# Optimization experiments

Hardware: AMD Instinct MI355X
Metric: run time of the kernel (lower is better)

Reference implementation:

```python
import jax, jax.numpy as jnp
import numpy as np

N = 1024       # sentence length (words incl. root at index 0)
WD = 300       # word embedding dim (GloVe-style)
PD = 25        # pos_emb_dim
H = 125        # hidden_dim_lstm
FC = 100       # hidden_dim_fc
PVOCAB = 50    # POS tagset size


def setup_inputs() -> dict:
    key = jax.random.key(0)
    ks = jax.random.split(key, 14)
    f = lambda k, s: jax.random.normal(k, s, dtype=jnp.float32) * 0.1
    d_in = WD + PD
    return {
        "word_vecs": jax.random.normal(ks[0], (N, WD), dtype=jnp.float32),
        "pos_idx": jax.random.randint(ks[1], (N,), 0, PVOCAB),
        "parents_ids": jax.random.randint(ks[2], (N,), 0, N),
        "pos_emb": f(ks[3], (PVOCAB, PD)),
        "Wih0": f(ks[4], (2, 4 * H, d_in)),
        "Whh0": f(ks[5], (2, 4 * H, H)),
        "b0": f(ks[6], (2, 4 * H)),
        "Wih1": f(ks[7], (2, 4 * H, 2 * H)),
        "Whh1": f(ks[8], (2, 4 * H, H)),
        "b1": f(ks[9], (2, 4 * H)),
        "fc1_W": f(ks[10], (FC, 4 * H)),
        "fc1_b": f(ks[11], (FC,)),
        "fc2_W": f(ks[12], (1, FC)),
        "fc2_b": f(ks[13], (1,)),
    }


def _lstm_dir(x, Wih, Whh, b, reverse):
    # torch LSTM cell, gate order (i, f, g, o); b = b_ih + b_hh
    Hd = Whh.shape[1]
    def step(carry, xt):
        h, c = carry
        g = xt @ Wih.T + h @ Whh.T + b
        i, fg, gg, o = jnp.split(g, 4)
        i = jax.nn.sigmoid(i)
        fg = jax.nn.sigmoid(fg)
        gg = jnp.tanh(gg)
        o = jax.nn.sigmoid(o)
        c = fg * c + i * gg
        h = o * jnp.tanh(c)
        return (h, c), h
    init = (jnp.zeros((Hd,), x.dtype), jnp.zeros((Hd,), x.dtype))
    _, hs = jax.lax.scan(step, init, x, reverse=reverse)
    return hs  # [n, H], already in original time order


def _bilstm_layer(x, Wih, Whh, b):
    hf = _lstm_dir(x, Wih[0], Whh[0], b[0], False)
    hb = _lstm_dir(x, Wih[1], Whh[1], b[1], True)
    return jnp.concatenate([hf, hb], axis=1)  # [n, 2H]


def reference(word_vecs, pos_idx, parents_ids, pos_emb, Wih0, Whh0, b0,
              Wih1, Whh1, b1, fc1_W, fc1_b, fc2_W, fc2_b):
    # encoder: concat word + pos embeddings, 2-layer BiLSTM
    x = jnp.concatenate([word_vecs, pos_emb[pos_idx]], axis=1)  # [n, WD+PD]
    h = _bilstm_layer(x, Wih0, Whh0, b0)
    h = _bilstm_layer(h, Wih1, Whh1, b1)  # [n, 2H]
    n = h.shape[0]
    twoH = h.shape[1]
    # fc1(cat(h_i, h_j)) = h_i @ W_head^T + h_j @ W_child^T + b  (vectorized over all pairs)
    A = h @ fc1_W[:, :twoH].T   # head contribution  [n, FC]
    B = h @ fc1_W[:, twoH:].T   # child contribution [n, FC]
    T = jnp.tanh(A[:, None, :] + B[None, :, :] + fc1_b)  # [n, n, FC]
    raw = T @ fc2_W[0] + fc2_b[0]                         # [n, n]
    ii = jnp.arange(n)
    # original loop skips diagonal and arcs into the root (j == 0); those stay 0
    mask = (ii[:, None] != ii[None, :]) & (ii[None, :] != 0)
    scores_mat = jnp.where(mask, raw, jnp.float32(0.0))
    logits = scores_mat.T  # row j = scores of heads for child j
    logp = jax.nn.log_softmax(logits, axis=1)
    loss = -jnp.mean(logp[jnp.arange(n), parents_ids])
    return loss, scores_mat
```

## Files before the change

kernel.cpp:

```cpp
#include <hip/hip_runtime.h>

typedef float v2f __attribute__((ext_vector_type(2)));

#define LOG2E 1.4426950408889634f
#define LN2   0.6931471805599453f

__device__ __forceinline__ float fexp2(float x) {
  float r; asm("v_exp_f32 %0, %1" : "=v"(r) : "v"(x)); return r;
}
__device__ __forceinline__ float frcp(float x) {
  float r; asm("v_rcp_f32 %0, %1" : "=v"(r) : "v"(x)); return r;
}
__device__ __forceinline__ float flog2(float x) {
  float r; asm("v_log_f32 %0, %1" : "=v"(r) : "v"(x)); return r;
}
__device__ __forceinline__ float dpp_xor1(float v) {
  return __builtin_bit_cast(float,
      __builtin_amdgcn_update_dpp(0, __builtin_bit_cast(int, v), 0xB1, 0xF, 0xF, true));
}
__device__ __forceinline__ float dpp_xor2(float v) {
  return __builtin_bit_cast(float,
      __builtin_amdgcn_update_dpp(0, __builtin_bit_cast(int, v), 0x4E, 0xF, 0xF, true));
}

__global__ void k_embed(const float* __restrict__ wv, const int* __restrict__ pidx,
                        const float* __restrict__ pemb, float* __restrict__ X) {
  int t = blockIdx.x;
  int pi = pidx[t];
  for (int c = threadIdx.x; c < 336; c += 128) {
    float v;
    if (c < 300)      v = wv[t * 300 + c];
    else if (c < 325) v = pemb[pi * 25 + (c - 300)];
    else              v = 0.f;
    X[t * 336 + c] = v;
  }
}

__global__ void k_repack(const float* __restrict__ src, float* __restrict__ dst,
                         int sK, int dK) {
  int r = blockIdx.x;
  for (int c = threadIdx.x; c < dK; c += 128)
    dst[r * dK + c] = (c < sK) ? src[r * sK + c] : 0.f;
}

__global__ void k_wab(const float* __restrict__ fc1W, float* __restrict__ Wab) {
  int r = blockIdx.x;
  int sr = (r < 100) ? r : r - 100;
  int so = (r < 100) ? 0 : 250;
  for (int c = threadIdx.x; c < 256; c += 128)
    Wab[r * 256 + c] = (c < 250) ? fc1W[sr * 500 + so + c] : 0.f;
}

__global__ void k_misc(const float* __restrict__ fc1b, const float* __restrict__ fc2W,
                       float* __restrict__ biasAB, float* __restrict__ sumw) {
  __shared__ float red[128];
  int t = threadIdx.x;
  for (int c = t; c < 256; c += 128)
    biasAB[c] = (c < 100) ? fc1b[c] : 0.f;
  float s = (t < 100) ? fc2W[t] : 0.f;
  red[t] = s; __syncthreads();
  for (int off = 64; off; off >>= 1) {
    if (t < off) red[t] += red[t + off];
    __syncthreads();
  }
  if (t == 0) sumw[0] = red[0];
}

#define BM 64
#define BN 64
#define BKK 16
__global__ __launch_bounds__(256) void k_gemm(
    const float* __restrict__ A, const float* __restrict__ Bw,
    const float* __restrict__ bias, float* __restrict__ C,
    int M, int N, int K, int ldC, long sBz, long sCz, long sbz, int transOut) {
  const int z = blockIdx.z;
  const float* Bp = Bw + (size_t)z * sBz;
  const float* bp = bias + (size_t)z * sbz;
  float* Cp = C + (size_t)z * sCz;
  const int bm = blockIdx.y * BM, bn = blockIdx.x * BN;
  __shared__ __align__(16) float As[BKK][BM + 4];
  __shared__ __align__(16) float Bs[BKK][BN + 4];
  __shared__ float Ts[BN][BM + 1];
  const int tid = threadIdx.x;
  const int tx = tid & 15, ty = tid >> 4;
  const int lr = tid >> 2;
  const int lk = (tid & 3) * 4;
  float acc[4][4];
#pragma unroll
  for (int a = 0; a < 4; ++a)
#pragma unroll
    for (int b = 0; b < 4; ++b) acc[a][b] = 0.f;

  int brow = bn + lr; if (brow >= N) brow = N - 1;
  for (int k0 = 0; k0 < K; k0 += BKK) {
    float4 a4 = *(const float4*)(A + (size_t)(bm + lr) * K + k0 + lk);
    float4 b4 = *(const float4*)(Bp + (size_t)brow * K + k0 + lk);
    __syncthreads();
    As[lk + 0][lr] = a4.x; As[lk + 1][lr] = a4.y; As[lk + 2][lr] = a4.z; As[lk + 3][lr] = a4.w;
    Bs[lk + 0][lr] = b4.x; Bs[lk + 1][lr] = b4.y; Bs[lk + 2][lr] = b4.z; Bs[lk + 3][lr] = b4.w;
    __syncthreads();
#pragma unroll
    for (int kk = 0; kk < BKK; ++kk) {
      float4 av = *(const float4*)&As[kk][ty * 4];
      float4 bv = *(const float4*)&Bs[kk][tx * 4];
      float aa[4] = {av.x, av.y, av.z, av.w};
      float bb[4] = {bv.x, bv.y, bv.z, bv.w};
#pragma unroll
      for (int a = 0; a < 4; ++a)
#pragma unroll
        for (int b = 0; b < 4; ++b)
          acc[a][b] = __builtin_fmaf(aa[a], bb[b], acc[a][b]);
    }
  }
  if (!transOut) {
#pragma unroll
    for (int a = 0; a < 4; ++a) {
      int i = bm + ty * 4 + a;
#pragma unroll
      for (int b = 0; b < 4; ++b) {
        int j = bn + tx * 4 + b;
        if (j < N) Cp[(size_t)i * ldC + j] = acc[a][b] + bp[j];
      }
    }
  } else {
    __syncthreads();
#pragma unroll
    for (int a = 0; a < 4; ++a)
#pragma unroll
      for (int b = 0; b < 4; ++b) {
        int jn = bn + tx * 4 + b; if (jn >= N) jn = N - 1;
        Ts[tx * 4 + b][ty * 4 + a] = acc[a][b] + bp[jn];
      }
    __syncthreads();
    const int n2 = tid >> 2, mq = (tid & 3) * 16;
    const int n = bn + n2;
    if (n < N) {
#pragma unroll
      for (int r = 0; r < 4; ++r) {
        int m0 = mq + r * 4;
        float4 v;
        v.x = Ts[n2][m0 + 0]; v.y = Ts[n2][m0 + 1];
        v.z = Ts[n2][m0 + 2]; v.w = Ts[n2][m0 + 3];
        *(float4*)(Cp + (size_t)n * ldC + bm + m0) = v;
      }
    }
  }
}

__global__ __launch_bounds__(512, 2) void k_rec(const float* __restrict__ Pt,
                                                const float* __restrict__ Whh,
                                                float* __restrict__ hout) {
  const int d = blockIdx.x;
  const bool fwd = (d == 0);
  const int t = threadIdx.x;
  int u = t >> 2; const bool active = (u < 125); if (u > 124) u = 124;
  const int sub = t & 3;

  const float* Wd = Whh + (size_t)d * 500 * 125;
  v2f w[4][16];
#pragma unroll
  for (int g = 0; g < 4; ++g) {
    const float* wr = Wd + (size_t)(g * 125 + u) * 125;
#pragma unroll
    for (int j = 0; j < 16; ++j) {
      int col = sub * 32 + 2 * j;
      v2f ww;
      ww.x = (col     < 125) ? wr[col]     : 0.f;
      ww.y = (col + 1 < 125) ? wr[col + 1] : 0.f;
      w[g][j] = ww;
    }
  }

  __shared__ __align__(16) float hb[2][160];
  __shared__ float hist[32][128];
  for (int i = t; i < 320; i += 512) ((float*)hb)[i] = 0.f;

  const int prow = sub * 125 + u;
  const float4* Pr = (const float4*)(Pt + (size_t)d * 500 * 1024 + (size_t)prow * 1024);

  const float sM = (sub == 2) ? 2.f : 1.f;
  const float sA = (sub == 2) ? 2.f : 1.f;
  const float sB = (sub == 2) ? -1.f : 0.f;
  const bool m0s = (sub == 0), m1s = (sub == 1), m2s = (sub == 2);

  float cst = 0.f;
  float4 cura = Pr[fwd ? 0 : 254];
  float4 curb = Pr[fwd ? 1 : 255];
  __syncthreads();

  for (int cb = 0; cb < 128; ++cb) {
    int nc = (cb + 1 < 128) ? cb + 1 : cb;
    float4 nxta = Pr[fwd ? 2 * nc     : 254 - 2 * nc];
    float4 nxtb = Pr[fwd ? 2 * nc + 1 : 255 - 2 * nc];
#pragma unroll
    for (int e = 0; e < 8; ++e) {
      const int buf = e & 1;
      float pf = (e == 0) ? cura.x : (e == 1) ? cura.y : (e == 2) ? cura.z : (e == 3) ? cura.w
               : (e == 4) ? curb.x : (e == 5) ? curb.y : (e == 6) ? curb.z : curb.w;
      float pb = (e == 0) ? curb.w : (e == 1) ? curb.z : (e == 2) ? curb.y : (e == 3) ? curb.x
               : (e == 4) ? cura.w : (e == 5) ? cura.z : (e == 6) ? cura.y : cura.x;
      float pre = fwd ? pf : pb;
      const float4* hp = (const float4*)&hb[buf][36 * sub];
      v2f a0 = {0.f, 0.f}, a1 = {0.f, 0.f}, a2 = {0.f, 0.f}, a3 = {0.f, 0.f};
#pragma unroll
      for (int q = 0; q < 8; ++q) {
        float4 hv = hp[q];
        v2f ha; ha.x = hv.x; ha.y = hv.y;
        v2f hc; hc.x = hv.z; hc.y = hv.w;
        a0 = __builtin_elementwise_fma(w[0][2 * q], ha, a0);
        a0 = __builtin_elementwise_fma(w[0][2 * q + 1], hc, a0);
        a1 = __builtin_elementwise_fma(w[1][2 * q], ha, a1);
        a1 = __builtin_elementwise_fma(w[1][2 * q + 1], hc, a1);
        a2 = __builtin_elementwise_fma(w[2][2 * q], ha, a2);
        a2 = __builtin_elementwise_fma(w[2][2 * q + 1], hc, a2);
        a3 = __builtin_elementwise_fma(w[3][2 * q], ha, a3);
        a3 = __builtin_elementwise_fma(w[3][2 * q + 1], hc, a3);
      }
      float p0 = a0.x + a0.y, p1 = a1.x + a1.y, p2 = a2.x + a2.y, p3 = a3.x + a3.y;
      p0 += dpp_xor1(p0); p0 += dpp_xor2(p0);
      p1 += dpp_xor1(p1); p1 += dpp_xor2(p1);
      p2 += dpp_xor1(p2); p2 += dpp_xor2(p2);
      p3 += dpp_xor1(p3); p3 += dpp_xor2(p3);
      float x = m0s ? p0 : m1s ? p1 : m2s ? p2 : p3;
      x += pre;
      float sg = frcp(1.f + fexp2(-LOG2E * (sM * x)));
      float a = __builtin_fmaf(sA, sg, sB);
      float fg = dpp_xor1(a);
      float gg = dpp_xor2(a);
      float og = dpp_xor2(fg);
      cst = __builtin_fmaf(fg, cst, a * gg);
      float th = __builtin_fmaf(2.f, frcp(1.f + fexp2(-2.f * LOG2E * cst)), -1.f);
      float h = og * th;
      if (m0s && active) {
        hb[buf ^ 1][u + 4 * (u >> 5)] = h;
        hist[(cb & 3) * 8 + e][u] = h;
      }
      __syncthreads();
    }
    if ((cb & 3) == 3) {
      const int S0 = (cb - 3) * 8;
#pragma unroll
      for (int k = 0; k < 8; ++k) {
        int idx = t + k * 512;
        int r = idx >> 7, u2 = idx & 127;
        if (u2 < 125) {
          int step = S0 + r;
          int time = fwd ? step : 1023 - step;
          hout[(size_t)time * 256 + d * 125 + u2] = hist[r][u2];
        }
      }
      __syncthreads();
    }
    cura = nxta; curb = nxtb;
  }
}

__global__ __launch_bounds__(256) void k_pair(const float* __restrict__ AB,
    const float* __restrict__ fc2W, const float* __restrict__ fc2b,
    const float* __restrict__ sumw, float* __restrict__ outS,
    float* __restrict__ scoresT) {
  __shared__ float As[32][100];
  __shared__ float Bs[32][101];
  __shared__ float w2s[100];
  const int tid = threadIdx.x;
  const int i0 = blockIdx.y * 32, j0 = blockIdx.x * 32;
  for (int idx = tid; idx < 3200; idx += 256) {
    int r = idx / 100, k = idx - r * 100;
    As[r][k] = AB[(size_t)(i0 + r) * 200 + k];
    Bs[r][k] = AB[(size_t)(j0 + r) * 200 + 100 + k];
  }
  if (tid < 100) w2s[tid] = 2.f * fc2W[tid];
  __syncthreads();
  const int tx = tid & 31, ty = tid >> 5;
  float acc[4] = {0.f, 0.f, 0.f, 0.f};
#pragma unroll 4
  for (int k = 0; k < 100; ++k) {
    float b = Bs[tx][k];
    float wk2 = w2s[k];
    float bs = b * (2.f * LOG2E);
#pragma unroll
    for (int q = 0; q < 4; ++q) {
      float a = As[ty + 8 * q][k];
      float r = frcp(1.f + fexp2(__builtin_fmaf(a, 2.f * LOG2E, bs)));
      acc[q] = __builtin_fmaf(wk2, r, acc[q]);
    }
  }
  float base = sumw[0] + fc2b[0];
  const int j = j0 + tx;
#pragma unroll
  for (int q = 0; q < 4; ++q) {
    int i = i0 + ty + 8 * q;
    float val = (i != j && j != 0) ? (base - acc[q]) : 0.f;
    outS[(size_t)i * 1024 + j] = val;
    scoresT[(size_t)j * 1024 + i] = val;
  }
}

__global__ __launch_bounds__(256) void k_soft(const float* __restrict__ scoresT,
    const int* __restrict__ parents, float* __restrict__ contrib) {
  const int j = blockIdx.x, tid = threadIdx.x;
  __shared__ float red[256];
  const float* row = scoresT + (size_t)j * 1024;
  float v0 = row[tid], v1 = row[tid + 256], v2 = row[tid + 512], v3 = row[tid + 768];
  float m = fmaxf(fmaxf(v0, v1), fmaxf(v2, v3));
  red[tid] = m; __syncthreads();
  for (int off = 128; off; off >>= 1) {
    if (tid < off) red[tid] = fmaxf(red[tid], red[tid + off]);
    __syncthreads();
  }
  m = red[0]; __syncthreads();
  float s = fexp2((v0 - m) * LOG2E) + fexp2((v1 - m) * LOG2E) +
            fexp2((v2 - m) * LOG2E) + fexp2((v3 - m) * LOG2E);
  red[tid] = s; __syncthreads();
  for (int off = 128; off; off >>= 1) {
    if (tid < off) red[tid] += red[tid + off];
    __syncthreads();
  }
  if (tid == 0) {
    float S = red[0];
    int p = parents[j];
    contrib[j] = row[p] - m - flog2(S) * LN2;
  }
}

__global__ __launch_bounds__(256) void k_loss(const float* __restrict__ contrib,
                                              float* __restrict__ out) {
  __shared__ float red[256];
  int tid = threadIdx.x;
  float s = contrib[tid] + contrib[tid + 256] + contrib[tid + 512] + contrib[tid + 768];
  red[tid] = s; __syncthreads();
  for (int off = 128; off; off >>= 1) {
    if (tid < off) red[tid] += red[tid + off];
    __syncthreads();
  }
  if (tid == 0) out[0] = -red[0] * (1.f / 1024.f);
}

extern "C" void kernel_launch(void* const* d_in, const int* in_sizes, int n_in,
                              void* d_out, int out_size, void* d_ws, size_t ws_size,
                              hipStream_t stream) {
  const float* wv   = (const float*)d_in[0];
  const int*   pidx = (const int*)d_in[1];
  const int*   par  = (const int*)d_in[2];
  const float* pemb = (const float*)d_in[3];
  const float* Wih0 = (const float*)d_in[4];
  const float* Whh0 = (const float*)d_in[5];
  const float* b0   = (const float*)d_in[6];
  const float* Wih1 = (const float*)d_in[7];
  const float* Whh1 = (const float*)d_in[8];
  const float* b1   = (const float*)d_in[9];
  const float* fc1W = (const float*)d_in[10];
  const float* fc1b = (const float*)d_in[11];
  const float* fc2W = (const float*)d_in[12];
  const float* fc2b = (const float*)d_in[13];
  float* ws = (float*)d_ws;
  float* X      = ws + 0;
  float* Wih0p  = ws + 344064;
  float* Pt0    = ws + 680064;
  float* h0     = ws + 1704064;
  float* Wih1p  = ws + 1966208;
  float* Pt1    = ws + 2222208;
  float* h1     = ws + 3246208;
  float* Wab    = ws + 3508352;
  float* biasAB = ws + 3559552;
  float* AB     = ws + 3559808;
  float* scT    = ws + 3764608;
  float* contrib= ws + 4813184;
  float* sumw   = ws + 4814208;
  float* out = (float*)d_out;

  hipMemsetAsync(h0, 0, 1024 * 256 * sizeof(float), stream);
  hipMemsetAsync(h1, 0, 1024 * 256 * sizeof(float), stream);

  k_embed <<<1024, 128, 0, stream>>>(wv, pidx, pemb, X);
  k_repack<<<1000, 128, 0, stream>>>(Wih0, Wih0p, 325, 336);
  k_repack<<<1000, 128, 0, stream>>>(Wih1, Wih1p, 250, 256);
  k_wab   <<<200, 128, 0, stream>>>(fc1W, Wab);
  k_misc  <<<1, 128, 0, stream>>>(fc1b, fc2W, biasAB, sumw);

  k_gemm<<<dim3(8, 16, 2), 256, 0, stream>>>(X, Wih0p, b0, Pt0, 1024, 500, 336, 1024,
                                             500L * 336, 500L * 1024, 500L, 1);
  k_rec <<<2, 512, 0, stream>>>(Pt0, Whh0, h0);
  k_gemm<<<dim3(8, 16, 2), 256, 0, stream>>>(h0, Wih1p, b1, Pt1, 1024, 500, 256, 1024,
                                             500L * 256, 500L * 1024, 500L, 1);
  k_rec <<<2, 512, 0, stream>>>(Pt1, Whh1, h1);
  k_gemm<<<dim3(4, 16, 1), 256, 0, stream>>>(h1, Wab, biasAB, AB, 1024, 200, 256, 200,
                                             0L, 0L, 0L, 0);
  k_pair<<<dim3(32, 32), 256, 0, stream>>>(AB, fc2W, fc2b, sumw, out + 1, scT);
  k_soft<<<1024, 256, 0, stream>>>(scT, par, contrib);
  k_loss<<<1, 256, 0, stream>>>(contrib, out);
}
```

Baseline: 1.350 ms.

## Shorten LSTM recurrence step: prescale gates, fused DPP reduce, lighter barriers

Folds the sigmoid/tanh log2e and gate-g factor-of-two scaling into Wih, Whh and the bias during preprocessing, so the serial per-step gate math skips a multiply. Replaces four separate butterfly reductions with a transpose-style DPP reduction that produces each lane's own gate sum in fewer cross-lane ops. Templates the loop on direction, uses inline v_pk_fma_f32, and swaps __syncthreads for an lgkmcnt-only wait plus s_barrier. This targets latency on the 1024-step sequential critical path, at the cost of relying on inline asm and a weaker barrier that only waits for LDS operations.

```diff
diff --git a/kernel.cpp b/kernel.cpp
--- a/kernel.cpp
+++ b/kernel.cpp
@@ -1,6 +1,7 @@
 #include <hip/hip_runtime.h>
 
 typedef float v2f __attribute__((ext_vector_type(2)));
+typedef float v4f __attribute__((ext_vector_type(4)));
 
 #define LOG2E 1.4426950408889634f
 #define LN2   0.6931471805599453f
@@ -13,6 +14,10 @@
 }
 __device__ __forceinline__ float flog2(float x) {
   float r; asm("v_log_f32 %0, %1" : "=v"(r) : "v"(x)); return r;
+}
+__device__ __forceinline__ v2f pkfma(v2f a, v2f b, v2f c) {
+  v2f d; asm("v_pk_fma_f32 %0, %1, %2, %3" : "=v"(d) : "v"(a), "v"(b), "v"(c));
+  return d;
 }
 __device__ __forceinline__ float dpp_xor1(float v) {
   return __builtin_bit_cast(float,
@@ -21,6 +26,9 @@
 __device__ __forceinline__ float dpp_xor2(float v) {
   return __builtin_bit_cast(float,
       __builtin_amdgcn_update_dpp(0, __builtin_bit_cast(int, v), 0x4E, 0xF, 0xF, true));
+}
+__device__ __forceinline__ void barrier_lgkm() {
+  asm volatile("s_waitcnt lgkmcnt(0)\n\ts_barrier" ::: "memory");
 }
 
 __global__ void k_embed(const float* __restrict__ wv, const int* __restrict__ pidx,
@@ -37,10 +45,20 @@
 }
 
 __global__ void k_repack(const float* __restrict__ src, float* __restrict__ dst,
-                         int sK, int dK) {
+                         int sK, int dK, int doScale) {
   int r = blockIdx.x;
+  float sc = 1.f;
+  if (doScale) { int gate = (r % 500) / 125; sc = (gate == 2) ? 2.f * LOG2E : LOG2E; }
   for (int c = threadIdx.x; c < dK; c += 128)
-    dst[r * dK + c] = (c < sK) ? src[r * sK + c] : 0.f;
+    dst[r * dK + c] = (c < sK) ? src[r * sK + c] * sc : 0.f;
+}
+
+__global__ void k_bscale(const float* __restrict__ b, float* __restrict__ bs) {
+  int i = blockIdx.x * 256 + threadIdx.x;
+  if (i < 1000) {
+    int gate = (i % 500) / 125;
+    bs[i] = b[i] * ((gate == 2) ? 2.f * LOG2E : LOG2E);
+  }
 }
 
 __global__ void k_wab(const float* __restrict__ fc1W, float* __restrict__ Wab) {
@@ -147,83 +165,54 @@
   }
 }
 
-__global__ __launch_bounds__(512, 2) void k_rec(const float* __restrict__ Pt,
-                                                const float* __restrict__ Whh,
-                                                float* __restrict__ hout) {
-  const int d = blockIdx.x;
-  const bool fwd = (d == 0);
-  const int t = threadIdx.x;
-  int u = t >> 2; const bool active = (u < 125); if (u > 124) u = 124;
-  const int sub = t & 3;
-
-  const float* Wd = Whh + (size_t)d * 500 * 125;
-  v2f w[4][16];
-#pragma unroll
-  for (int g = 0; g < 4; ++g) {
-    const float* wr = Wd + (size_t)(g * 125 + u) * 125;
-#pragma unroll
-    for (int j = 0; j < 16; ++j) {
-      int col = sub * 32 + 2 * j;
-      v2f ww;
-      ww.x = (col     < 125) ? wr[col]     : 0.f;
-      ww.y = (col + 1 < 125) ? wr[col + 1] : 0.f;
-      w[g][j] = ww;
-    }
-  }
-
-  __shared__ __align__(16) float hb[2][160];
-  __shared__ float hist[32][128];
-  for (int i = t; i < 320; i += 512) ((float*)hb)[i] = 0.f;
-
-  const int prow = sub * 125 + u;
-  const float4* Pr = (const float4*)(Pt + (size_t)d * 500 * 1024 + (size_t)prow * 1024);
-
-  const float sM = (sub == 2) ? 2.f : 1.f;
-  const float sA = (sub == 2) ? 2.f : 1.f;
-  const float sB = (sub == 2) ? -1.f : 0.f;
-  const bool m0s = (sub == 0), m1s = (sub == 1), m2s = (sub == 2);
-
+template<bool FWD>
+__device__ __forceinline__ void rec_loop(
+    const float4* __restrict__ Pr, const v2f (&w)[4][16],
+    float (*hb)[160], float (*hist)[128],
+    float* __restrict__ hout, int d, int t, int u, int sub, bool active,
+    float sA, float sB) {
+  const bool b1s = (sub & 1) != 0;
+  const bool b2s = (sub & 2) != 0;
+  const bool wr = (sub == 0) && active;
   float cst = 0.f;
-  float4 cura = Pr[fwd ? 0 : 254];
-  float4 curb = Pr[fwd ? 1 : 255];
-  __syncthreads();
+  float4 cura = Pr[FWD ? 0 : 254];
+  float4 curb = Pr[FWD ? 1 : 255];
+  barrier_lgkm();
 
   for (int cb = 0; cb < 128; ++cb) {
     int nc = (cb + 1 < 128) ? cb + 1 : cb;
-    float4 nxta = Pr[fwd ? 2 * nc     : 254 - 2 * nc];
-    float4 nxtb = Pr[fwd ? 2 * nc + 1 : 255 - 2 * nc];
+    float4 nxta = Pr[FWD ? 2 * nc     : 254 - 2 * nc];
+    float4 nxtb = Pr[FWD ? 2 * nc + 1 : 255 - 2 * nc];
 #pragma unroll
     for (int e = 0; e < 8; ++e) {
       const int buf = e & 1;
-      float pf = (e == 0) ? cura.x : (e == 1) ? cura.y : (e == 2) ? cura.z : (e == 3) ? cura.w
-               : (e == 4) ? curb.x : (e == 5) ? curb.y : (e == 6) ? curb.z : curb.w;
-      float pb = (e == 0) ? curb.w : (e == 1) ? curb.z : (e == 2) ? curb.y : (e == 3) ? curb.x
-               : (e == 4) ? cura.w : (e == 5) ? cura.z : (e == 6) ? cura.y : cura.x;
-      float pre = fwd ? pf : pb;
-      const float4* hp = (const float4*)&hb[buf][36 * sub];
+      float pre;
+      if (FWD)
+        pre = (e == 0) ? cura.x : (e == 1) ? cura.y : (e == 2) ? cura.z : (e == 3) ? cura.w
+            : (e == 4) ? curb.x : (e == 5) ? curb.y : (e == 6) ? curb.z : curb.w;
+      else
+        pre = (e == 0) ? curb.w : (e == 1) ? curb.z : (e == 2) ? curb.y : (e == 3) ? curb.x
+            : (e == 4) ? cura.w : (e == 5) ? cura.z : (e == 6) ? cura.y : cura.x;
+      const v4f* hp = (const v4f*)&hb[buf][36 * sub];
       v2f a0 = {0.f, 0.f}, a1 = {0.f, 0.f}, a2 = {0.f, 0.f}, a3 = {0.f, 0.f};
 #pragma unroll
       for (int q = 0; q < 8; ++q) {
-        float4 hv = hp[q];
-        v2f ha; ha.x = hv.x; ha.y = hv.y;
-        v2f hc; hc.x = hv.z; hc.y = hv.w;
-        a0 = __builtin_elementwise_fma(w[0][2 * q], ha, a0);
-        a0 = __builtin_elementwise_fma(w[0][2 * q + 1], hc, a0);
-        a1 = __builtin_elementwise_fma(w[1][2 * q], ha, a1);
-        a1 = __builtin_elementwise_fma(w[1][2 * q + 1], hc, a1);
-        a2 = __builtin_elementwise_fma(w[2][2 * q], ha, a2);
-        a2 = __builtin_elementwise_fma(w[2][2 * q + 1], hc, a2);
-        a3 = __builtin_elementwise_fma(w[3][2 * q], ha, a3);
-        a3 = __builtin_elementwise_fma(w[3][2 * q + 1], hc, a3);
+        v4f hv = hp[q];
+        v2f ha = __builtin_shufflevector(hv, hv, 0, 1);
+        v2f hc = __builtin_shufflevector(hv, hv, 2, 3);
+        a0 = pkfma(w[0][2 * q], ha, a0); a0 = pkfma(w[0][2 * q + 1], hc, a0);
+        a1 = pkfma(w[1][2 * q], ha, a1); a1 = pkfma(w[1][2 * q + 1], hc, a1);
+        a2 = pkfma(w[2][2 * q], ha, a2); a2 = pkfma(w[2][2 * q + 1], hc, a2);
+        a3 = pkfma(w[3][2 * q], ha, a3); a3 = pkfma(w[3][2 * q + 1], hc, a3);
       }
       float p0 = a0.x + a0.y, p1 = a1.x + a1.y, p2 = a2.x + a2.y, p3 = a3.x + a3.y;
-      p0 += dpp_xor1(p0); p0 += dpp_xor2(p0);
-      p1 += dpp_xor1(p1); p1 += dpp_xor2(p1);
-      p2 += dpp_xor1(p2); p2 += dpp_xor2(p2);
-      p3 += dpp_xor1(p3); p3 += dpp_xor2(p3);
-      float x = m0s ? p0 : m1s ? p1 : m2s ? p2 : p3;
-      x += pre;
-      float sg = frcp(1.f + fexp2(-LOG2E * (sM * x)));
+      float s01 = b1s ? p0 : p1, k01 = b1s ? p1 : p0;
+      float r01 = k01 + dpp_xor1(s01);
+      float s23 = b1s ? p2 : p3, k23 = b1s ? p3 : p2;
+      float r23 = k23 + dpp_xor1(s23);
+      float sv = b2s ? r01 : r23, kv = b2s ? r23 : r01;
+      float x = kv + dpp_xor2(sv) + pre;
+      float sg = frcp(1.f + fexp2(-x));
       float a = __builtin_fmaf(sA, sg, sB);
       float fg = dpp_xor1(a);
       float gg = dpp_xor2(a);
@@ -231,11 +220,11 @@
       cst = __builtin_fmaf(fg, cst, a * gg);
       float th = __builtin_fmaf(2.f, frcp(1.f + fexp2(-2.f * LOG2E * cst)), -1.f);
       float h = og * th;
-      if (m0s && active) {
+      if (wr) {
         hb[buf ^ 1][u + 4 * (u >> 5)] = h;
         hist[(cb & 3) * 8 + e][u] = h;
       }
-      __syncthreads();
+      barrier_lgkm();
     }
     if ((cb & 3) == 3) {
       const int S0 = (cb - 3) * 8;
@@ -245,14 +234,51 @@
         int r = idx >> 7, u2 = idx & 127;
         if (u2 < 125) {
           int step = S0 + r;
-          int time = fwd ? step : 1023 - step;
+          int time = FWD ? step : 1023 - step;
           hout[(size_t)time * 256 + d * 125 + u2] = hist[r][u2];
         }
       }
-      __syncthreads();
+      barrier_lgkm();
     }
     cura = nxta; curb = nxtb;
   }
+}
+
+__global__ __launch_bounds__(512, 2) void k_rec(const float* __restrict__ Pt,
+                                                const float* __restrict__ Whh,
+                                                float* __restrict__ hout) {
+  const int d = blockIdx.x;
+  const int t = threadIdx.x;
+  int u = t >> 2; const bool active = (u < 125); if (u > 124) u = 124;
+  const int sub = t & 3;
+
+  const float* Wd = Whh + (size_t)d * 500 * 125;
+  v2f w[4][16];
+#pragma unroll
+  for (int g = 0; g < 4; ++g) {
+    const float sc = (g == 2) ? 2.f * LOG2E : LOG2E;
+    const float* wrp = Wd + (size_t)(g * 125 + u) * 125;
+#pragma unroll
+    for (int j = 0; j < 16; ++j) {
+      int col = sub * 32 + 2 * j;
+      v2f ww;
+      ww.x = (col     < 125) ? wrp[col]     * sc : 0.f;
+      ww.y = (col + 1 < 125) ? wrp[col + 1] * sc : 0.f;
+      w[g][j] = ww;
+    }
+  }
+
+  __shared__ __align__(16) float hb[2][160];
+  __shared__ float hist[32][128];
+  for (int i = t; i < 320; i += 512) ((float*)hb)[i] = 0.f;
+
+  const int prow = sub * 125 + u;
+  const float4* Pr = (const float4*)(Pt + (size_t)d * 500 * 1024 + (size_t)prow * 1024);
+  const float sA = (sub == 2) ? 2.f : 1.f;
+  const float sB = (sub == 2) ? -1.f : 0.f;
+
+  if (d == 0) rec_loop<true >(Pr, w, hb, hist, hout, d, t, u, sub, active, sA, sB);
+  else        rec_loop<false>(Pr, w, hb, hist, hout, d, t, u, sub, active, sA, sB);
 }
 
 __global__ __launch_bounds__(256) void k_pair(const float* __restrict__ AB,
@@ -367,21 +393,25 @@
   float* scT    = ws + 3764608;
   float* contrib= ws + 4813184;
   float* sumw   = ws + 4814208;
+  float* bs0    = ws + 4814212;
+  float* bs1    = ws + 4815212;
   float* out = (float*)d_out;
 
   hipMemsetAsync(h0, 0, 1024 * 256 * sizeof(float), stream);
   hipMemsetAsync(h1, 0, 1024 * 256 * sizeof(float), stream);
 
   k_embed <<<1024, 128, 0, stream>>>(wv, pidx, pemb, X);
-  k_repack<<<1000, 128, 0, stream>>>(Wih0, Wih0p, 325, 336);
-  k_repack<<<1000, 128, 0, stream>>>(Wih1, Wih1p, 250, 256);
+  k_repack<<<1000, 128, 0, stream>>>(Wih0, Wih0p, 325, 336, 1);
+  k_repack<<<1000, 128, 0, stream>>>(Wih1, Wih1p, 250, 256, 1);
+  k_bscale<<<4, 256, 0, stream>>>(b0, bs0);
+  k_bscale<<<4, 256, 0, stream>>>(b1, bs1);
   k_wab   <<<200, 128, 0, stream>>>(fc1W, Wab);
   k_misc  <<<1, 128, 0, stream>>>(fc1b, fc2W, biasAB, sumw);
 
-  k_gemm<<<dim3(8, 16, 2), 256, 0, stream>>>(X, Wih0p, b0, Pt0, 1024, 500, 336, 1024,
+  k_gemm<<<dim3(8, 16, 2), 256, 0, stream>>>(X, Wih0p, bs0, Pt0, 1024, 500, 336, 1024,
                                              500L * 336, 500L * 1024, 500L, 1);
   k_rec <<<2, 512, 0, stream>>>(Pt0, Whh0, h0);
-  k_gemm<<<dim3(8, 16, 2), 256, 0, stream>>>(h0, Wih1p, b1, Pt1, 1024, 500, 256, 1024,
+  k_gemm<<<dim3(8, 16, 2), 256, 0, stream>>>(h0, Wih1p, bs1, Pt1, 1024, 500, 256, 1024,
                                              500L * 256, 500L * 1024, 500L, 1);
   k_rec <<<2, 512, 0, stream>>>(Pt1, Whh1, h1);
   k_gemm<<<dim3(4, 16, 1), 256, 0, stream>>>(h1, Wab, biasAB, AB, 1024, 200, 256, 200,
```

Result: no change. 1.354 ms (+0.3%).
